# Kernel tuning notes

Hardware: AMD Instinct MI355X
Metric: run time of the kernel (lower is better)

## Reference

```python
import jax, jax.numpy as jnp
import numpy as np

B, T, W_DIM = 32, 2048, 1024
G, D = 16, 64          # num_groups, input_dim (w = G*D)
MOM = 0.9
TH = 0.5
EPS = 1e-8
TOP_K = 2


def setup_inputs() -> dict:
    key = jax.random.key(0)
    k = jax.random.split(key, 4)
    x = jax.random.normal(k[0], (B, T, W_DIM), dtype=jnp.float32)
    ema = jnp.zeros((W_DIM, W_DIM), dtype=jnp.float32)
    W1 = jax.random.normal(k[1], (G, 16, D), dtype=jnp.float32) * 0.05
    b1 = jnp.zeros((G, 16), dtype=jnp.float32)
    W2 = jax.random.normal(k[2], (G, 1, 16), dtype=jnp.float32) * 0.05
    b2 = jnp.zeros((G, 1), dtype=jnp.float32)
    return {"x": x, "ema": ema, "W1": W1, "b1": b1, "W2": W2, "b2": b2}


def _corr_over_T(x):
    # x: (B, T, w) -> per-batch Pearson corr over the T axis: (B, w, w)
    Tn = x.shape[1]
    c = x - x.mean(axis=1, keepdims=True)
    cov = jnp.einsum('btw,btv->bwv', c, c) / (Tn - 1)
    std = jnp.sqrt(jnp.sum(c * c, axis=1) / (Tn - 1))  # (B, w)
    return jnp.clip(cov / (std[:, :, None] * std[:, None, :] + EPS), -1.0, 1.0)


def reference(x, ema, W1, b1, W2, b2):
    # --- burst-masked EMA update (torch.no_grad) ---
    corr_batch = jax.lax.stop_gradient(_corr_over_T(x))  # (B, w, w)

    def step(e, c):
        mask = jnp.abs(c) > TH
        return jnp.where(mask, MOM * e + (1.0 - MOM) * c, e), None

    ema_new, _ = jax.lax.scan(step, ema, corr_batch)

    # --- split into groups: (B, T, G, D) ---
    Bn, Tn, w = x.shape
    groups = x.reshape(Bn, Tn, G, D)

    # --- per-group correlation score: mean |off-diagonal| of within-group corr ---
    cg = groups - groups.mean(axis=1, keepdims=True)
    cov_g = jnp.einsum('btgd,btge->bgde', cg, cg) / (Tn - 1)        # (B, G, D, D)
    std_g = jnp.sqrt(jnp.sum(cg * cg, axis=1) / (Tn - 1))           # (B, G, D)
    corr_g = jnp.clip(cov_g / (std_g[..., :, None] * std_g[..., None, :] + EPS), -1.0, 1.0)
    absc = jnp.abs(corr_g)
    offdiag = (absc.sum(axis=(-2, -1)) - jnp.einsum('bgdd->bg', absc)) / (D * D - D)
    correlations = offdiag.mean(axis=0)                              # (G,)

    # --- select the 2 least-correlated groups (these get gradients) ---
    _, sel = jax.lax.top_k(-correlations, TOP_K)
    sel_mask = jnp.zeros((G,), dtype=bool).at[sel].set(True)

    # --- per-group expert MLP: D -> 16 -> 1, batched over groups ---
    h = jax.nn.relu(jnp.einsum('btgd,ghd->btgh', groups, W1) + b1)   # (B, T, G, 16)
    o = (jnp.einsum('btgh,goh->btgo', h, W2) + b2)[..., 0]           # (B, T, G)

    # non-selected groups run under no_grad -> stop_gradient on their outputs
    out = jnp.where(sel_mask[None, None, :], o, jax.lax.stop_gradient(o))
    return out, correlations, ema_new
```

## Files before the change

### kernel.cpp

```cpp
#include <hip/hip_runtime.h>
#include <hip/hip_bf16.h>
#include <stdint.h>

#define B_   32
#define T_   2048
#define W_   1024
#define G_   16
#define D_   64
#define LIST_CAP 65536
#define BK   32

typedef __bf16 bf16_t;
typedef __bf16 bf16x8 __attribute__((ext_vector_type(8)));
typedef float  f32x4  __attribute__((ext_vector_type(4)));

#define WS_XT      0ull
#define WS_XT_SZ   (134217728ull)
#define WS_SUM     (WS_XT + WS_XT_SZ)
#define WS_SQ      (WS_SUM + 131072ull)
#define WS_MU      (WS_SQ  + 131072ull)
#define WS_SIG     (WS_MU  + 131072ull)
#define WS_ACCUM   (WS_SIG + 131072ull)
#define WS_LISTCNT (WS_ACCUM + 256ull)
#define WS_LIST    (WS_LISTCNT + 256ull)
#define WS_MASK    (WS_LIST + 1048576ull)
#define WS_DIAG    (WS_MASK + 4194304ull)

__global__ __launch_bounds__(256) void stats_transpose(
    const float* __restrict__ x, bf16_t* __restrict__ xT,
    float* __restrict__ sumb, float* __restrict__ sqb) {
  int b = blockIdx.z, t0 = blockIdx.x * 64, w0 = blockIdx.y * 64;
  __shared__ float tile[64][65];
  __shared__ float rs[64][17], rq[64][17];
  int tid = threadIdx.x;
  int wc = tid & 15, tr = tid >> 4;
  float4 s4 = {0.f, 0.f, 0.f, 0.f}, q4 = {0.f, 0.f, 0.f, 0.f};
  const float4* xp = (const float4*)(x + ((size_t)b * T_ + t0) * W_ + w0);
#pragma unroll
  for (int p = 0; p < 4; ++p) {
    int t = tr + 16 * p;
    float4 v = xp[(size_t)t * 256 + wc];
    s4.x += v.x; s4.y += v.y; s4.z += v.z; s4.w += v.w;
    q4.x += v.x * v.x; q4.y += v.y * v.y; q4.z += v.z * v.z; q4.w += v.w * v.w;
    tile[4 * wc + 0][t] = v.x;
    tile[4 * wc + 1][t] = v.y;
    tile[4 * wc + 2][t] = v.z;
    tile[4 * wc + 3][t] = v.w;
  }
  rs[4 * wc + 0][tr] = s4.x; rs[4 * wc + 1][tr] = s4.y;
  rs[4 * wc + 2][tr] = s4.z; rs[4 * wc + 3][tr] = s4.w;
  rq[4 * wc + 0][tr] = q4.x; rq[4 * wc + 1][tr] = q4.y;
  rq[4 * wc + 2][tr] = q4.z; rq[4 * wc + 3][tr] = q4.w;
  __syncthreads();
  if (tid < 64) {
    float s = 0.f, q = 0.f;
#pragma unroll
    for (int i = 0; i < 16; ++i) { s += rs[tid][i]; q += rq[tid][i]; }
    atomicAdd(&sumb[b * W_ + w0 + tid], s);
    atomicAdd(&sqb[b * W_ + w0 + tid], q);
  }
  int c = tid & 7, wv = tid >> 3;
#pragma unroll
  for (int p = 0; p < 2; ++p) {
    int w = wv + 32 * p;
    const float* src = &tile[w][c * 8];
    bf16x8 o;
#pragma unroll
    for (int k = 0; k < 8; ++k) o[k] = (bf16_t)src[k];
    *(bf16x8*)(xT + ((size_t)b * W_ + w0 + w) * T_ + t0 + c * 8) = o;
  }
}

__global__ void finalize_stats(const float* __restrict__ sumb,
                               const float* __restrict__ sqb,
                               float* __restrict__ mu, float* __restrict__ sig) {
  int idx = blockIdx.x * 256 + threadIdx.x;
  float s = sumb[idx], q = sqb[idx];
  float m = s * (1.0f / 2048.0f);
  float var = (q - s * m) * (1.0f / 2047.0f);
  if (var < 0.f) var = 0.f;
  mu[idx] = m;
  sig[idx] = sqrtf(var);
}

__global__ __launch_bounds__(256) void gram_kernel(
    const bf16_t* __restrict__ xT, const float* __restrict__ mu,
    const float* __restrict__ sig, unsigned int* __restrict__ mask,
    float* __restrict__ diagv, int* __restrict__ listcnt,
    int4* __restrict__ list, float* __restrict__ accum) {
  int id = blockIdx.x;
  int xcd = id & 7;
  int idx = id >> 3;
  int sub = idx / 36;
  int rt  = idx % 36;
  int b = sub * 8 + xcd;
  int r = rt, ti = 0;
  while (r >= 8 - ti) { r -= 8 - ti; ++ti; }
  int tj = ti + r;
  int i0 = ti * 128, j0 = tj * 128;

  const bf16_t* Ag = xT + ((size_t)b * W_ + i0) * T_;
  const bf16_t* Bg = xT + ((size_t)b * W_ + j0) * T_;

  __shared__ __attribute__((aligned(16))) bf16_t As[3][128 * BK];
  __shared__ __attribute__((aligned(16))) bf16_t Bs[3][128 * BK];

  int tid = threadIdx.x;
  int lane = tid & 63, wave = tid >> 6;
  int wm = wave >> 1, wn = wave & 1;

  auto stage = [&](int buf, int k0) {
    bf16_t* Ad = &As[buf][0];
    bf16_t* Bd = &Bs[buf][0];
#pragma unroll
    for (int s = 0; s < 2; ++s) {
      int c = s * 256 + tid;
      int row = c >> 2, slot = c & 3;
      int gslot = slot ^ ((row >> 1) & 3);
      __builtin_amdgcn_global_load_lds(
          (const __attribute__((address_space(1))) void*)(Ag + (size_t)row * T_ + k0 + gslot * 8),
          (__attribute__((address_space(3))) void*)(Ad + c * 8), 16, 0, 0);
      __builtin_amdgcn_global_load_lds(
          (const __attribute__((address_space(1))) void*)(Bg + (size_t)row * T_ + k0 + gslot * 8),
          (__attribute__((address_space(3))) void*)(Bd + c * 8), 16, 0, 0);
    }
  };

  f32x4 zero = {0.f, 0.f, 0.f, 0.f};
  f32x4 acc[4][4];
#pragma unroll
  for (int mi = 0; mi < 4; ++mi)
#pragma unroll
    for (int nj = 0; nj < 4; ++nj) acc[mi][nj] = zero;

  int arow = wm * 64 + (lane & 15);
  int brow = wn * 64 + (lane & 15);
  int q = lane >> 4;

  stage(0, 0);
  stage(1, BK);

  const int NT = T_ / BK;
#pragma unroll 1
  for (int kt = 0; kt < NT; ++kt) {
    int cur = kt % 3;
    if (kt < NT - 1) {
      asm volatile("s_waitcnt vmcnt(4)" ::: "memory");
    } else {
      asm volatile("s_waitcnt vmcnt(0)" ::: "memory");
    }
    __builtin_amdgcn_s_barrier();

    const bf16_t* Ac = &As[cur][0];
    const bf16_t* Bc = &Bs[cur][0];
    bf16x8 af[4], bfr[4];
#pragma unroll
    for (int mi = 0; mi < 4; ++mi) {
      int row = arow + mi * 16;
      af[mi] = *(const bf16x8*)(Ac + row * BK + (q ^ ((row >> 1) & 3)) * 8);
    }
#pragma unroll
    for (int nj = 0; nj < 4; ++nj) {
      int row = brow + nj * 16;
      bfr[nj] = *(const bf16x8*)(Bc + row * BK + (q ^ ((row >> 1) & 3)) * 8);
    }
#pragma unroll
    for (int mi = 0; mi < 4; ++mi)
#pragma unroll
      for (int nj = 0; nj < 4; ++nj)
        acc[mi][nj] = __builtin_amdgcn_mfma_f32_16x16x32_bf16(af[mi], bfr[nj], acc[mi][nj], 0, 0, 0);

    if (kt < NT - 2) stage((kt + 2) % 3, (kt + 2) * BK);
  }

  const float inv = 1.0f / 2047.0f;
  const float* mub = mu + b * W_;
  const float* sgb = sig + b * W_;
  bool diagquad = (ti == tj) && (wm == wn);
  float gsum = 0.f;

#pragma unroll
  for (int nj = 0; nj < 4; ++nj) {
    int j = j0 + wn * 64 + nj * 16 + (lane & 15);
    float muj = mub[j], sgj = sgb[j];
#pragma unroll
    for (int mi = 0; mi < 4; ++mi) {
#pragma unroll
      for (int rr = 0; rr < 4; ++rr) {
        int i = i0 + wm * 64 + mi * 16 + (lane >> 4) * 4 + rr;
        float cov = (acc[mi][nj][rr] - 2048.0f * mub[i] * muj) * inv;
        float corr = cov / (sgb[i] * sgj + 1e-8f);
        corr = fminf(1.0f, fmaxf(-1.0f, corr));
        if (diagquad && (i != j)) gsum += fabsf(corr);
        if (fabsf(corr) > 0.5f) {
          atomicOr(&mask[i * W_ + j], 1u << b);
          if (i == j) {
            diagv[b * W_ + i] = corr;
          } else {
            int p = atomicAdd(listcnt, 1);
            if (p < LIST_CAP) list[p] = make_int4(b, i, j, __float_as_int(corr));
          }
          if (ti != tj) {
            atomicOr(&mask[j * W_ + i], 1u << b);
            int p = atomicAdd(listcnt, 1);
            if (p < LIST_CAP) list[p] = make_int4(b, j, i, __float_as_int(corr));
          }
        }
      }
    }
  }
  if (diagquad) {
    for (int o = 32; o > 0; o >>= 1) gsum += __shfl_down(gsum, o);
    if (lane == 0) atomicAdd(&accum[ti * 2 + wm], gsum);
  }
}

__global__ void ema_kernel(const float* __restrict__ ema,
                           const unsigned int* __restrict__ mask,
                           const float* __restrict__ diagv,
                           const int* __restrict__ listcnt,
                           const int4* __restrict__ list,
                           float* __restrict__ emaout) {
  int idx = blockIdx.x * 256 + threadIdx.x;
  int i = idx >> 10, j = idx & 1023;
  float e = ema[idx];
  unsigned int m = mask[idx];
  if (m) {
    if (i == j) {
      for (int b = 0; b < 32; ++b)
        if ((m >> b) & 1u) e = 0.9f * e + 0.1f * diagv[b * W_ + i];
    } else {
      int cnt = *listcnt; if (cnt > LIST_CAP) cnt = LIST_CAP;
      for (int b = 0; b < 32; ++b) {
        if ((m >> b) & 1u) {
          for (int k = 0; k < cnt; ++k) {
            int4 t = list[k];
            if (t.x == b && t.y == i && t.z == j) {
              e = 0.9f * e + 0.1f * __int_as_float(t.w);
              break;
            }
          }
        }
      }
    }
  }
  emaout[idx] = e;
}

__global__ void corr_finalize(const float* __restrict__ accum, float* __restrict__ outc) {
  int g = threadIdx.x;
  if (g < 16) outc[g] = accum[g] * (1.0f / (32.0f * 4032.0f));
}

__global__ __launch_bounds__(256) void mlp_kernel(
    const float* __restrict__ x, const float* __restrict__ W1,
    const float* __restrict__ b1, const float* __restrict__ W2,
    const float* __restrict__ b2, float* __restrict__ out) {
  int b = blockIdx.y, t0 = blockIdx.x * 256, gs = blockIdx.z * 4;
  int tid = threadIdx.x;
  int gl = tid & 3, tl = tid >> 2;
  __shared__ __attribute__((aligned(16))) float Wt[4 * 1092 + 16];
  __shared__ float b1s[16 * 4], W2s[16 * 4], b2s[4];
  for (int l = tid; l < 4096; l += 256) {
    int g2 = l >> 10, r = l & 1023;
    int j = r >> 6, d = r & 63;
    Wt[g2 * 1092 + j * 68 + d] = W1[(size_t)(gs + g2) * 1024 + r];
  }
  if (tid < 64) {
    int g2 = tid & 3, j = tid >> 2;
    b1s[j * 4 + g2] = b1[(gs + g2) * 16 + j];
    W2s[j * 4 + g2] = W2[(gs + g2) * 16 + j];
  }
  if (tid < 4) b2s[tid] = b2[gs + tid];
  __syncthreads();

  int g = gs + gl;
  const float* xb = x + ((size_t)b * T_ + t0 + tl) * W_ + g * D_;
  const float* wbase = &Wt[gl * 1092];
  float h0[16], h1[16], h2[16], h3[16];
#pragma unroll
  for (int j = 0; j < 16; ++j) {
    float bj = b1s[j * 4 + gl];
    h0[j] = bj; h1[j] = bj; h2[j] = bj; h3[j] = bj;
  }
#pragma unroll
  for (int d4 = 0; d4 < 16; ++d4) {
    float4 x0 = *(const float4*)(xb + 0 * 64 * W_ + d4 * 4);
    float4 x1 = *(const float4*)(xb + 1 * 64 * W_ + d4 * 4);
    float4 x2 = *(const float4*)(xb + 2 * 64 * W_ + d4 * 4);
    float4 x3 = *(const float4*)(xb + 3 * 64 * W_ + d4 * 4);
#pragma unroll
    for (int j = 0; j < 16; ++j) {
      float4 wv = *(const float4*)(wbase + j * 68 + d4 * 4);
      h0[j] += x0.x * wv.x + x0.y * wv.y + x0.z * wv.z + x0.w * wv.w;
      h1[j] += x1.x * wv.x + x1.y * wv.y + x1.z * wv.z + x1.w * wv.w;
      h2[j] += x2.x * wv.x + x2.y * wv.y + x2.z * wv.z + x2.w * wv.w;
      h3[j] += x3.x * wv.x + x3.y * wv.y + x3.z * wv.z + x3.w * wv.w;
    }
  }
  size_t ob = ((size_t)b * T_ + t0 + tl) * 16 + g;
  float o0 = b2s[gl], o1 = b2s[gl], o2 = b2s[gl], o3 = b2s[gl];
#pragma unroll
  for (int j = 0; j < 16; ++j) {
    float w2 = W2s[j * 4 + gl];
    o0 += fmaxf(h0[j], 0.f) * w2;
    o1 += fmaxf(h1[j], 0.f) * w2;
    o2 += fmaxf(h2[j], 0.f) * w2;
    o3 += fmaxf(h3[j], 0.f) * w2;
  }
  out[ob + 0 * 64 * 16] = o0;
  out[ob + 1 * 64 * 16] = o1;
  out[ob + 2 * 64 * 16] = o2;
  out[ob + 3 * 64 * 16] = o3;
}

extern "C" void kernel_launch(void* const* d_in, const int* in_sizes, int n_in,
                              void* d_out, int out_size, void* d_ws, size_t ws_size,
                              hipStream_t stream) {
  const float* x   = (const float*)d_in[0];
  const float* ema = (const float*)d_in[1];
  const float* W1  = (const float*)d_in[2];
  const float* b1  = (const float*)d_in[3];
  const float* W2  = (const float*)d_in[4];
  const float* b2  = (const float*)d_in[5];

  float* out    = (float*)d_out;
  float* outc   = out + 1048576;
  float* outema = outc + 16;

  char* ws = (char*)d_ws;
  bf16_t* xT        = (bf16_t*)(ws + WS_XT);
  float* sumb       = (float*)(ws + WS_SUM);
  float* sqb        = (float*)(ws + WS_SQ);
  float* mub        = (float*)(ws + WS_MU);
  float* sigb       = (float*)(ws + WS_SIG);
  float* accum      = (float*)(ws + WS_ACCUM);
  int*   listcnt    = (int*)(ws + WS_LISTCNT);
  int4*  list       = (int4*)(ws + WS_LIST);
  unsigned int* msk = (unsigned int*)(ws + WS_MASK);
  float* diagv      = (float*)(ws + WS_DIAG);

  hipMemsetAsync(ws + WS_SUM, 0, 262144, stream);
  hipMemsetAsync(ws + WS_ACCUM, 0, 512, stream);
  hipMemsetAsync(ws + WS_MASK, 0, 4194304, stream);

  stats_transpose<<<dim3(32, 16, 32), 256, 0, stream>>>(x, xT, sumb, sqb);
  finalize_stats<<<128, 256, 0, stream>>>(sumb, sqb, mub, sigb);
  gram_kernel<<<1152, 256, 0, stream>>>(xT, mub, sigb, msk, diagv, listcnt, list, accum);
  ema_kernel<<<4096, 256, 0, stream>>>(ema, msk, diagv, listcnt, list, outema);
  corr_finalize<<<1, 16, 0, stream>>>(accum, outc);
  mlp_kernel<<<dim3(8, 32, 4), 256, 0, stream>>>(x, W1, b1, W2, b2, out);
}
```

Baseline: 697.1 us.

## Give each wave its own 64x64 upper-triangle tile, loading fragments straight from global into registers

```diff
diff --git a/kernel.cpp b/kernel.cpp
--- a/kernel.cpp
+++ b/kernel.cpp
@@ -90,108 +90,81 @@
     int4* __restrict__ list, float* __restrict__ accum) {
   int id = blockIdx.x;
   int xcd = id & 7;
-  int idx = id >> 3;
-  int sub = idx / 36;
-  int rt  = idx % 36;
+  int rest = id >> 3;
+  int sub = rest / 34;
+  int r34 = rest % 34;
   int b = sub * 8 + xcd;
-  int r = rt, ti = 0;
-  while (r >= 8 - ti) { r -= 8 - ti; ++ti; }
-  int tj = ti + r;
-  int i0 = ti * 128, j0 = tj * 128;
-
-  const bf16_t* Ag = xT + ((size_t)b * W_ + i0) * T_;
-  const bf16_t* Bg = xT + ((size_t)b * W_ + j0) * T_;
-
-  __shared__ __attribute__((aligned(16))) bf16_t As[3][128 * BK];
-  __shared__ __attribute__((aligned(16))) bf16_t Bs[3][128 * BK];
 
   int tid = threadIdx.x;
   int lane = tid & 63, wave = tid >> 6;
-  int wm = wave >> 1, wn = wave & 1;
-
-  auto stage = [&](int buf, int k0) {
-    bf16_t* Ad = &As[buf][0];
-    bf16_t* Bd = &Bs[buf][0];
-#pragma unroll
-    for (int s = 0; s < 2; ++s) {
-      int c = s * 256 + tid;
-      int row = c >> 2, slot = c & 3;
-      int gslot = slot ^ ((row >> 1) & 3);
-      __builtin_amdgcn_global_load_lds(
-          (const __attribute__((address_space(1))) void*)(Ag + (size_t)row * T_ + k0 + gslot * 8),
-          (__attribute__((address_space(3))) void*)(Ad + c * 8), 16, 0, 0);
-      __builtin_amdgcn_global_load_lds(
-          (const __attribute__((address_space(1))) void*)(Bg + (size_t)row * T_ + k0 + gslot * 8),
-          (__attribute__((address_space(3))) void*)(Bd + c * 8), 16, 0, 0);
+  int task = r34 * 4 + wave;
+  int rr_ = task, pi = 0;
+  while (rr_ >= 16 - pi) { rr_ -= 16 - pi; ++pi; }
+  int pj = pi + rr_;
+  int i0 = pi * 64, j0 = pj * 64;
+
+  int frow = lane & 15;
+  int q = lane >> 4;
+
+  const bf16_t* Abase = xT + ((size_t)b * W_ + i0 + frow) * T_ + q * 8;
+  const bf16_t* Bbase = xT + ((size_t)b * W_ + j0 + frow) * T_ + q * 8;
+
+  f32x4 zero = {0.f, 0.f, 0.f, 0.f};
+  f32x4 acc[4][4];
+#pragma unroll
+  for (int mi = 0; mi < 4; ++mi)
+#pragma unroll
+    for (int nj = 0; nj < 4; ++nj) acc[mi][nj] = zero;
+
+  bf16x8 a0[4], b0[4], a1[4], b1[4];
+
+  auto loadAB = [&](bf16x8* Af, bf16x8* Bf, int kt) {
+#pragma unroll
+    for (int mi = 0; mi < 4; ++mi) {
+      Af[mi] = *(const bf16x8*)(Abase + (size_t)mi * 16 * T_ + kt * BK);
+      Bf[mi] = *(const bf16x8*)(Bbase + (size_t)mi * 16 * T_ + kt * BK);
     }
   };
-
-  f32x4 zero = {0.f, 0.f, 0.f, 0.f};
-  f32x4 acc[4][4];
-#pragma unroll
-  for (int mi = 0; mi < 4; ++mi)
-#pragma unroll
-    for (int nj = 0; nj < 4; ++nj) acc[mi][nj] = zero;
-
-  int arow = wm * 64 + (lane & 15);
-  int brow = wn * 64 + (lane & 15);
-  int q = lane >> 4;
-
-  stage(0, 0);
-  stage(1, BK);
+  auto mfmaAB = [&](const bf16x8* Aq, const bf16x8* Bq) {
+#pragma unroll
+    for (int mi = 0; mi < 4; ++mi)
+#pragma unroll
+      for (int nj = 0; nj < 4; ++nj)
+        acc[mi][nj] = __builtin_amdgcn_mfma_f32_16x16x32_bf16(Aq[mi], Bq[nj], acc[mi][nj], 0, 0, 0);
+  };
 
   const int NT = T_ / BK;
+  loadAB(a0, b0, 0);
+  loadAB(a1, b1, 1);
 #pragma unroll 1
-  for (int kt = 0; kt < NT; ++kt) {
-    int cur = kt % 3;
-    if (kt < NT - 1) {
-      asm volatile("s_waitcnt vmcnt(4)" ::: "memory");
-    } else {
-      asm volatile("s_waitcnt vmcnt(0)" ::: "memory");
-    }
-    __builtin_amdgcn_s_barrier();
-
-    const bf16_t* Ac = &As[cur][0];
-    const bf16_t* Bc = &Bs[cur][0];
-    bf16x8 af[4], bfr[4];
-#pragma unroll
-    for (int mi = 0; mi < 4; ++mi) {
-      int row = arow + mi * 16;
-      af[mi] = *(const bf16x8*)(Ac + row * BK + (q ^ ((row >> 1) & 3)) * 8);
-    }
-#pragma unroll
-    for (int nj = 0; nj < 4; ++nj) {
-      int row = brow + nj * 16;
-      bfr[nj] = *(const bf16x8*)(Bc + row * BK + (q ^ ((row >> 1) & 3)) * 8);
-    }
-#pragma unroll
-    for (int mi = 0; mi < 4; ++mi)
-#pragma unroll
-      for (int nj = 0; nj < 4; ++nj)
-        acc[mi][nj] = __builtin_amdgcn_mfma_f32_16x16x32_bf16(af[mi], bfr[nj], acc[mi][nj], 0, 0, 0);
-
-    if (kt < NT - 2) stage((kt + 2) % 3, (kt + 2) * BK);
-  }
+  for (int kt = 0; kt < NT - 2; kt += 2) {
+    mfmaAB(a0, b0);
+    loadAB(a0, b0, kt + 2);
+    mfmaAB(a1, b1);
+    loadAB(a1, b1, kt + 3);
+  }
+  mfmaAB(a0, b0);
+  mfmaAB(a1, b1);
 
   const float inv = 1.0f / 2047.0f;
   const float* mub = mu + b * W_;
   const float* sgb = sig + b * W_;
-  bool diagquad = (ti == tj) && (wm == wn);
+  bool diagpanel = (pi == pj);
   float gsum = 0.f;
 
 #pragma unroll
   for (int nj = 0; nj < 4; ++nj) {
-    int j = j0 + wn * 64 + nj * 16 + (lane & 15);
+    int j = j0 + nj * 16 + frow;
     float muj = mub[j], sgj = sgb[j];
 #pragma unroll
     for (int mi = 0; mi < 4; ++mi) {
 #pragma unroll
       for (int rr = 0; rr < 4; ++rr) {
-        int i = i0 + wm * 64 + mi * 16 + (lane >> 4) * 4 + rr;
+        int i = i0 + mi * 16 + q * 4 + rr;
         float cov = (acc[mi][nj][rr] - 2048.0f * mub[i] * muj) * inv;
         float corr = cov / (sgb[i] * sgj + 1e-8f);
         corr = fminf(1.0f, fmaxf(-1.0f, corr));
-        if (diagquad && (i != j)) gsum += fabsf(corr);
+        if (diagpanel && (i != j)) gsum += fabsf(corr);
         if (fabsf(corr) > 0.5f) {
           atomicOr(&mask[i * W_ + j], 1u << b);
           if (i == j) {
@@ -200,7 +173,7 @@
             int p = atomicAdd(listcnt, 1);
             if (p < LIST_CAP) list[p] = make_int4(b, i, j, __float_as_int(corr));
           }
-          if (ti != tj) {
+          if (pi != pj) {
             atomicOr(&mask[j * W_ + i], 1u << b);
             int p = atomicAdd(listcnt, 1);
             if (p < LIST_CAP) list[p] = make_int4(b, j, i, __float_as_int(corr));
@@ -209,9 +182,9 @@
       }
     }
   }
-  if (diagquad) {
+  if (diagpanel) {
     for (int o = 32; o > 0; o >>= 1) gsum += __shfl_down(gsum, o);
-    if (lane == 0) atomicAdd(&accum[ti * 2 + wm], gsum);
+    if (lane == 0) atomicAdd(&accum[pi], gsum);
   }
 }
 
@@ -346,7 +319,7 @@
 
   stats_transpose<<<dim3(32, 16, 32), 256, 0, stream>>>(x, xT, sumb, sqb);
   finalize_stats<<<128, 256, 0, stream>>>(sumb, sqb, mub, sigb);
-  gram_kernel<<<1152, 256, 0, stream>>>(xT, mub, sigb, msk, diagv, listcnt, list, accum);
+  gram_kernel<<<1088, 256, 0, stream>>>(xT, mub, sigb, msk, diagv, listcnt, list, accum);
   ema_kernel<<<4096, 256, 0, stream>>>(ema, msk, diagv, listcnt, list, outema);
   corr_finalize<<<1, 16, 0, stream>>>(accum, outc);
   mlp_kernel<<<dim3(8, 32, 4), 256, 0, stream>>>(x, W1, b1, W2, b2, out);
```

New measurement: 813.1 us. 1.17x slower.

## Enlarge Gram tiles to 256x256 full grid with BK=64 double buffering

Applied to the files above, without the earlier changes.

```diff
diff --git a/kernel.cpp b/kernel.cpp
--- a/kernel.cpp
+++ b/kernel.cpp
@@ -8,7 +8,7 @@
 #define G_   16
 #define D_   64
 #define LIST_CAP 65536
-#define BK   32
+#define BK   64
 
 typedef __bf16 bf16_t;
 typedef __bf16 bf16x8 __attribute__((ext_vector_type(8)));
@@ -83,40 +83,38 @@
   sig[idx] = sqrtf(var);
 }
 
-__global__ __launch_bounds__(256) void gram_kernel(
+__global__ __launch_bounds__(512) void gram_kernel(
     const bf16_t* __restrict__ xT, const float* __restrict__ mu,
     const float* __restrict__ sig, unsigned int* __restrict__ mask,
     float* __restrict__ diagv, int* __restrict__ listcnt,
     int4* __restrict__ list, float* __restrict__ accum) {
   int id = blockIdx.x;
   int xcd = id & 7;
-  int idx = id >> 3;
-  int sub = idx / 36;
-  int rt  = idx % 36;
+  int loc = id >> 3;
+  int sub = loc >> 4;
+  int tl  = loc & 15;
+  int ti = tl >> 2, tj = tl & 3;
   int b = sub * 8 + xcd;
-  int r = rt, ti = 0;
-  while (r >= 8 - ti) { r -= 8 - ti; ++ti; }
-  int tj = ti + r;
-  int i0 = ti * 128, j0 = tj * 128;
+  int i0 = ti * 256, j0 = tj * 256;
 
   const bf16_t* Ag = xT + ((size_t)b * W_ + i0) * T_;
   const bf16_t* Bg = xT + ((size_t)b * W_ + j0) * T_;
 
-  __shared__ __attribute__((aligned(16))) bf16_t As[3][128 * BK];
-  __shared__ __attribute__((aligned(16))) bf16_t Bs[3][128 * BK];
+  __shared__ __attribute__((aligned(16))) bf16_t As[2][256 * BK];
+  __shared__ __attribute__((aligned(16))) bf16_t Bs[2][256 * BK];
 
   int tid = threadIdx.x;
   int lane = tid & 63, wave = tid >> 6;
-  int wm = wave >> 1, wn = wave & 1;
+  int wm = wave >> 2, wn = wave & 3;
 
   auto stage = [&](int buf, int k0) {
     bf16_t* Ad = &As[buf][0];
     bf16_t* Bd = &Bs[buf][0];
 #pragma unroll
-    for (int s = 0; s < 2; ++s) {
-      int c = s * 256 + tid;
-      int row = c >> 2, slot = c & 3;
-      int gslot = slot ^ ((row >> 1) & 3);
+    for (int s = 0; s < 4; ++s) {
+      int c = s * 512 + tid;
+      int row = c >> 3, slot = c & 7;
+      int gslot = slot ^ (row & 7);
       __builtin_amdgcn_global_load_lds(
           (const __attribute__((address_space(1))) void*)(Ag + (size_t)row * T_ + k0 + gslot * 8),
           (__attribute__((address_space(3))) void*)(Ad + c * 8), 16, 0, 0);
@@ -127,56 +125,60 @@
   };
 
   f32x4 zero = {0.f, 0.f, 0.f, 0.f};
-  f32x4 acc[4][4];
-#pragma unroll
-  for (int mi = 0; mi < 4; ++mi)
+  f32x4 acc[8][4];
+#pragma unroll
+  for (int mi = 0; mi < 8; ++mi)
 #pragma unroll
     for (int nj = 0; nj < 4; ++nj) acc[mi][nj] = zero;
 
-  int arow = wm * 64 + (lane & 15);
+  int arow = wm * 128 + (lane & 15);
   int brow = wn * 64 + (lane & 15);
   int q = lane >> 4;
 
   stage(0, 0);
-  stage(1, BK);
 
   const int NT = T_ / BK;
 #pragma unroll 1
   for (int kt = 0; kt < NT; ++kt) {
-    int cur = kt % 3;
-    if (kt < NT - 1) {
-      asm volatile("s_waitcnt vmcnt(4)" ::: "memory");
+    int cur = kt & 1;
+    if (kt + 1 < NT) {
+      stage(cur ^ 1, (kt + 1) * BK);
+      asm volatile("s_waitcnt vmcnt(8)" ::: "memory");
     } else {
       asm volatile("s_waitcnt vmcnt(0)" ::: "memory");
     }
     __builtin_amdgcn_s_barrier();
+    __builtin_amdgcn_sched_barrier(0);
 
     const bf16_t* Ac = &As[cur][0];
     const bf16_t* Bc = &Bs[cur][0];
-    bf16x8 af[4], bfr[4];
-#pragma unroll
-    for (int mi = 0; mi < 4; ++mi) {
-      int row = arow + mi * 16;
-      af[mi] = *(const bf16x8*)(Ac + row * BK + (q ^ ((row >> 1) & 3)) * 8);
-    }
-#pragma unroll
-    for (int nj = 0; nj < 4; ++nj) {
-      int row = brow + nj * 16;
-      bfr[nj] = *(const bf16x8*)(Bc + row * BK + (q ^ ((row >> 1) & 3)) * 8);
-    }
-#pragma unroll
-    for (int mi = 0; mi < 4; ++mi)
-#pragma unroll
-      for (int nj = 0; nj < 4; ++nj)
-        acc[mi][nj] = __builtin_amdgcn_mfma_f32_16x16x32_bf16(af[mi], bfr[nj], acc[mi][nj], 0, 0, 0);
-
-    if (kt < NT - 2) stage((kt + 2) % 3, (kt + 2) * BK);
+#pragma unroll
+    for (int s2 = 0; s2 < 2; ++s2) {
+      bf16x8 af[8], bfr[4];
+#pragma unroll
+      for (int mi = 0; mi < 8; ++mi) {
+        int row = arow + mi * 16;
+        af[mi] = *(const bf16x8*)(Ac + row * BK + ((s2 * 4 + q) ^ (row & 7)) * 8);
+      }
+#pragma unroll
+      for (int nj = 0; nj < 4; ++nj) {
+        int row = brow + nj * 16;
+        bfr[nj] = *(const bf16x8*)(Bc + row * BK + ((s2 * 4 + q) ^ (row & 7)) * 8);
+      }
+#pragma unroll
+      for (int mi = 0; mi < 8; ++mi)
+#pragma unroll
+        for (int nj = 0; nj < 4; ++nj)
+          acc[mi][nj] = __builtin_amdgcn_mfma_f32_16x16x32_bf16(af[mi], bfr[nj], acc[mi][nj], 0, 0, 0);
+    }
+    asm volatile("s_waitcnt lgkmcnt(0)" ::: "memory");
+    __builtin_amdgcn_sched_barrier(0);
+    __builtin_amdgcn_s_barrier();
   }
 
   const float inv = 1.0f / 2047.0f;
   const float* mub = mu + b * W_;
   const float* sgb = sig + b * W_;
-  bool diagquad = (ti == tj) && (wm == wn);
   float gsum = 0.f;
 
 #pragma unroll
@@ -184,14 +186,14 @@
     int j = j0 + wn * 64 + nj * 16 + (lane & 15);
     float muj = mub[j], sgj = sgb[j];
 #pragma unroll
-    for (int mi = 0; mi < 4; ++mi) {
+    for (int mi = 0; mi < 8; ++mi) {
 #pragma unroll
       for (int rr = 0; rr < 4; ++rr) {
-        int i = i0 + wm * 64 + mi * 16 + (lane >> 4) * 4 + rr;
+        int i = i0 + wm * 128 + mi * 16 + q * 4 + rr;
         float cov = (acc[mi][nj][rr] - 2048.0f * mub[i] * muj) * inv;
         float corr = cov / (sgb[i] * sgj + 1e-8f);
         corr = fminf(1.0f, fmaxf(-1.0f, corr));
-        if (diagquad && (i != j)) gsum += fabsf(corr);
+        if (((i >> 6) == (j >> 6)) && (i != j)) gsum += fabsf(corr);
         if (fabsf(corr) > 0.5f) {
           atomicOr(&mask[i * W_ + j], 1u << b);
           if (i == j) {
@@ -200,18 +202,13 @@
             int p = atomicAdd(listcnt, 1);
             if (p < LIST_CAP) list[p] = make_int4(b, i, j, __float_as_int(corr));
           }
-          if (ti != tj) {
-            atomicOr(&mask[j * W_ + i], 1u << b);
-            int p = atomicAdd(listcnt, 1);
-            if (p < LIST_CAP) list[p] = make_int4(b, j, i, __float_as_int(corr));
-          }
         }
       }
     }
   }
-  if (diagquad) {
+  if ((ti == tj) && ((wn >> 1) == wm)) {
     for (int o = 32; o > 0; o >>= 1) gsum += __shfl_down(gsum, o);
-    if (lane == 0) atomicAdd(&accum[ti * 2 + wm], gsum);
+    if (lane == 0) atomicAdd(&accum[tj * 4 + wn], gsum);
   }
 }
 
@@ -346,7 +343,7 @@
 
   stats_transpose<<<dim3(32, 16, 32), 256, 0, stream>>>(x, xT, sumb, sqb);
   finalize_stats<<<128, 256, 0, stream>>>(sumb, sqb, mub, sigb);
-  gram_kernel<<<1152, 256, 0, stream>>>(xT, mub, sigb, msk, diagv, listcnt, list, accum);
+  gram_kernel<<<512, 512, 0, stream>>>(xT, mub, sigb, msk, diagv, listcnt, list, accum);
   ema_kernel<<<4096, 256, 0, stream>>>(ema, msk, diagv, listcnt, list, outema);
   corr_finalize<<<1, 16, 0, stream>>>(accum, outc);
   mlp_kernel<<<dim3(8, 32, 4), 256, 0, stream>>>(x, W1, b1, W2, b2, out);
```

New measurement: 692.7 us. About the same (-0.6%).
